# Kernel optimization log

Hardware: AMD Instinct MI355X
Metric: run time of the kernel (lower is better)

The kernel has to match this reference:

```python
import jax, jax.numpy as jnp
import numpy as np

NUM_HEADS = 16
HEAD_DIM = 64
WINDOW = 512
D_MODEL = NUM_HEADS * HEAD_DIM
BATCH = 2
SEQ = 2048


def setup_inputs() -> dict:
    key = jax.random.key(0)
    k1, k2, k3 = jax.random.split(key, 3)
    x = jax.random.normal(k1, (BATCH, SEQ, D_MODEL), dtype=jnp.float32)
    # Dense layer params (lecun_normal-like scale for stability)
    qkv_kernel = jax.random.normal(k2, (D_MODEL, 3 * NUM_HEADS * HEAD_DIM), dtype=jnp.float32) / np.sqrt(D_MODEL)
    qkv_bias = jnp.zeros((3 * NUM_HEADS * HEAD_DIM,), dtype=jnp.float32)
    out_kernel = jax.random.normal(k3, (NUM_HEADS * HEAD_DIM, D_MODEL), dtype=jnp.float32) / np.sqrt(D_MODEL)
    out_bias = jnp.zeros((D_MODEL,), dtype=jnp.float32)
    return {"x": x, "qkv_kernel": qkv_kernel, "qkv_bias": qkv_bias,
            "out_kernel": out_kernel, "out_bias": out_bias}


def reference(x, qkv_kernel, qkv_bias, out_kernel, out_bias):
    b, s, d = x.shape
    qkv = x @ qkv_kernel + qkv_bias                       # (b, s, 3*H*hd)
    qkv = qkv.reshape(b, s, 3, NUM_HEADS, HEAD_DIM)
    q = qkv[:, :, 0].transpose(0, 2, 1, 3)                # (b, H, s, hd)
    k = qkv[:, :, 1].transpose(0, 2, 1, 3)
    v = qkv[:, :, 2].transpose(0, 2, 1, 3)
    scale = 1.0 / jnp.sqrt(jnp.float32(HEAD_DIM)).astype(x.dtype)
    scores = jnp.einsum('bhqd,bhkd->bhqk', q, k) * scale  # (b, H, s, s)
    rows = jnp.arange(s)[:, None]
    cols = jnp.arange(s)[None, :]
    window_mask = (rows - cols >= 0) & (rows - cols < WINDOW)
    scores = jnp.where(window_mask[None, None], scores, jnp.asarray(-1e9, scores.dtype))
    attn = jax.nn.softmax(scores, axis=-1)
    out = jnp.einsum('bhqk,bhkd->bhqd', attn, v)          # (b, H, s, hd)
    out = out.transpose(0, 2, 1, 3).reshape(b, s, -1)
    return out @ out_kernel + out_bias
```

## Files before the change

kernel.cpp:

```cpp
#include <hip/hip_runtime.h>
#include <cstdint>
#include <cstddef>

#define NUM_HEADS 16
#define HEAD_DIM  64
#define WINDOW    512
#define D_MODEL   1024
#define BATCH     2
#define SEQ       2048
#define MTOT      (BATCH*SEQ)
#define NQKV      (3*D_MODEL)

typedef short bf16x8 __attribute__((ext_vector_type(8)));
typedef float f32x4  __attribute__((ext_vector_type(4)));

__device__ __forceinline__ f32x4 mfma16(bf16x8 a, bf16x8 b, f32x4 c) {
  return __builtin_amdgcn_mfma_f32_16x16x32_bf16(a, b, c, 0, 0, 0);
}

__device__ __forceinline__ unsigned short f2bf(float f) {
  unsigned int u = __float_as_uint(f);
  u += 0x7fffu + ((u >> 16) & 1u);
  return (unsigned short)(u >> 16);
}
__device__ __forceinline__ float bf2f(unsigned short b) {
  return __uint_as_float(((unsigned int)b) << 16);
}

__device__ __forceinline__ void gld16(const unsigned short* g, unsigned short* l) {
  __builtin_amdgcn_global_load_lds(
      (const __attribute__((address_space(1))) unsigned int*)g,
      (__attribute__((address_space(3))) unsigned int*)l, 16, 0, 0);
}

__global__ __launch_bounds__(256) void prep_kernel(const float* __restrict__ x,
                                                   const float* __restrict__ qkv_w,
                                                   const float* __restrict__ out_w,
                                                   unsigned short* __restrict__ Xb,
                                                   unsigned short* __restrict__ Wq,
                                                   unsigned short* __restrict__ Wo) {
  __shared__ float tile[32][33];
  const int bid = blockIdx.x, t = threadIdx.x;
  if (bid < 4096) {
    int i = (bid * 256 + t) * 4;
    float4 v = *(const float4*)(x + i);
    ushort4 o;
    o.x = f2bf(v.x); o.y = f2bf(v.y); o.z = f2bf(v.z); o.w = f2bf(v.w);
    *(ushort4*)(Xb + i) = o;
    return;
  }
  const float* in; unsigned short* out; int R, C, bx, by;
  if (bid < 7168) { int b2 = bid - 4096; in = qkv_w; out = Wq; R = D_MODEL; C = NQKV; bx = b2 % 96; by = b2 / 96; }
  else            { int b2 = bid - 7168; in = out_w; out = Wo; R = D_MODEL; C = D_MODEL; bx = b2 & 31; by = b2 >> 5; }
  int tx = t & 31, ty = t >> 5;
  int c0 = bx * 32, r0 = by * 32;
#pragma unroll
  for (int i = 0; i < 32; i += 8)
    tile[ty + i][tx] = in[(size_t)(r0 + ty + i) * C + c0 + tx];
  __syncthreads();
#pragma unroll
  for (int i = 0; i < 32; i += 8)
    out[(size_t)(c0 + ty + i) * R + r0 + tx] = f2bf(tile[tx][ty + i]);
}

template<bool SWAP, int K>
__device__ __forceinline__ void gemm_mainloop512(const unsigned short* __restrict__ A,
                                                 const unsigned short* __restrict__ Bt,
                                                 int m0, int n0,
                                                 unsigned short* sA, unsigned short* sB,
                                                 f32x4 (&acc)[2][4]) {
  const int t = threadIdx.x;
  const int lane = t & 63, wave = t >> 6;
  const int wr = wave >> 1, wc = wave & 1;
  const int lhi = lane >> 4, llo = lane & 15;
  f32x4 zero = {0.f, 0.f, 0.f, 0.f};
#pragma unroll
  for (int i = 0; i < 2; ++i)
#pragma unroll
    for (int j = 0; j < 4; ++j) acc[i][j] = zero;

  const int cswz = (((t & 3) ^ ((t >> 3) & 3)) << 3);
  const unsigned short* gA = A  + (size_t)(m0 + (t >> 2)) * K + cswz;
  const unsigned short* gB = Bt + (size_t)(n0 + (t >> 2)) * K + cswz;
  const int ldsT = t * 8;
  const int rsw  = (lhi ^ ((llo >> 1) & 3)) * 8;
  const int aoff = (wr * 32 + llo) * 32 + rsw;
  const int boff = (wc * 64 + llo) * 32 + rsw;
  constexpr int nIter = K / 32;

  auto stage = [&](int s) {
    unsigned short* dA = sA + (s % 3) * 4096;
    unsigned short* dB = sB + (s % 3) * 4096;
    gld16(gA + s * 32, dA + ldsT);
    gld16(gB + s * 32, dB + ldsT);
  };

  stage(0);
  stage(1);
#pragma unroll
  for (int it = 0; it < nIter; ++it) {
    if (it + 1 < nIter) asm volatile("s_waitcnt vmcnt(2)\n\ts_barrier" ::: "memory");
    else                asm volatile("s_waitcnt vmcnt(0)\n\ts_barrier" ::: "memory");
    if (it + 2 < nIter) stage(it + 2);
    const unsigned short* cA = sA + (it % 3) * 4096;
    const unsigned short* cB = sB + (it % 3) * 4096;
    bf16x8 af[2], bfr[4];
#pragma unroll
    for (int i = 0; i < 2; ++i) af[i]  = *(const bf16x8*)(cA + aoff + i * 512);
#pragma unroll
    for (int j = 0; j < 4; ++j)  bfr[j] = *(const bf16x8*)(cB + boff + j * 512);
#pragma unroll
    for (int i = 0; i < 2; ++i)
#pragma unroll
      for (int j = 0; j < 4; ++j)
        acc[i][j] = SWAP ? mfma16(bfr[j], af[i], acc[i][j])
                         : mfma16(af[i], bfr[j], acc[i][j]);
  }
}

__global__ __launch_bounds__(512, 6) void qkv_gemm_kernel(const unsigned short* __restrict__ Xb,
                                                          const unsigned short* __restrict__ Wt,
                                                          const float* __restrict__ bias,
                                                          unsigned short* __restrict__ Qw,
                                                          unsigned short* __restrict__ Kw,
                                                          unsigned short* __restrict__ Vtw) {
  __shared__ __align__(16) unsigned short sA[3][128 * 32];
  __shared__ __align__(16) unsigned short sB[3][128 * 32];
  f32x4 acc[2][4];
  const int m0 = blockIdx.y * 128, n0 = blockIdx.x * 128;
  const int t = threadIdx.x, lane = t & 63, wave = t >> 6;
  const int wr = wave >> 1, wc = wave & 1, lhi = lane >> 4, llo = lane & 15;

  if (n0 < 2048) {
    gemm_mainloop512<false, D_MODEL>(Xb, Wt, m0, n0, sA[0], sB[0], acc);
    const int c = n0 >> 10;
    unsigned short* __restrict__ Dst = (c == 0) ? Qw : Kw;
    const float qs = (c == 0) ? 0.125f : 1.0f;
#pragma unroll
    for (int ti = 0; ti < 2; ++ti) {
#pragma unroll
      for (int tj = 0; tj < 4; ++tj) {
        int n = n0 + wc * 64 + tj * 16 + llo;
        float bv = bias[n];
        int h = (n >> 6) & 15, d = n & 63;
#pragma unroll
        for (int r = 0; r < 4; ++r) {
          int m = m0 + wr * 32 + ti * 16 + lhi * 4 + r;
          int b = m >> 11, s = m & 2047;
          int bh = b * 16 + h;
          Dst[((size_t)(bh * 2048 + s)) * 64 + d] = f2bf((acc[ti][tj][r] + bv) * qs);
        }
      }
    }
  } else {
    gemm_mainloop512<true, D_MODEL>(Xb, Wt, m0, n0, sA[0], sB[0], acc);
#pragma unroll
    for (int ti = 0; ti < 2; ++ti) {
      int m = m0 + wr * 32 + ti * 16 + llo;
      int b = m >> 11, s = m & 2047;
#pragma unroll
      for (int tj = 0; tj < 4; ++tj) {
        int nb = n0 + wc * 64 + tj * 16 + lhi * 4;
        float4 bv = *(const float4*)(bias + nb);
        int h = (nb >> 6) & 15, dbase = nb & 63;
        int bh = b * 16 + h;
        float bvr[4] = {bv.x, bv.y, bv.z, bv.w};
#pragma unroll
        for (int r = 0; r < 4; ++r)
          Vtw[(size_t)(bh * 64 + dbase + r) * 2048 + s] = f2bf(acc[ti][tj][r] + bvr[r]);
      }
    }
  }
}

__global__ __launch_bounds__(512) void attn_kernel(const unsigned short* __restrict__ Qw,
                                                   const unsigned short* __restrict__ Kw,
                                                   const unsigned short* __restrict__ Vtw,
                                                   unsigned short* __restrict__ AO) {
  __shared__ __align__(16) unsigned short sK[3][64 * 64];
  __shared__ __align__(16) unsigned short sV[3][64 * 64];
  __shared__ __align__(16) unsigned short sP[8][16 * 72];
  const int t = threadIdx.x, lane = t & 63, wave = t >> 6;
  const int lhi = lane >> 4, llo = lane & 15;
  const int bh = blockIdx.x;
  const int q0 = (15 - blockIdx.y) << 7;
  const unsigned short* Qb = Qw  + (size_t)bh * 2048 * 64;
  const unsigned short* Kb = Kw  + (size_t)bh * 2048 * 64;
  const unsigned short* Vb = Vtw + (size_t)bh * 64 * 2048;

  const int qw = q0 + wave * 16;
  const int qrow = qw + llo;
  bf16x8 qf0 = *(const bf16x8*)(Qb + (size_t)qrow * 64 + lhi * 8);
  bf16x8 qf1 = *(const bf16x8*)(Qb + (size_t)qrow * 64 + 32 + lhi * 8);

  const int srow = t >> 3;
  const int scol = ((t & 7) ^ (srow & 7)) * 8;
  const int cpos  = (lhi ^ (llo & 7)) * 8;
  const int cposx = cpos ^ 32;

  float m_i = -1e30f, l_i = 0.f;
  f32x4 o[4];
  f32x4 zero = {0.f, 0.f, 0.f, 0.f};
#pragma unroll
  for (int td = 0; td < 4; ++td) o[td] = zero;

  const int kt_lo = (q0 > 511) ? ((q0 - 511) >> 6) : 0;
  const int kt_hi = (q0 + 127) >> 6;

  auto stageKV = [&](int j) {
    const int k0 = j << 6;
    unsigned short* dK = sK[j % 3];
    unsigned short* dV = sV[j % 3];
    gld16(Kb + (size_t)(k0 + srow) * 64 + scol, dK + t * 8);
    gld16(Vb + (size_t)srow * 2048 + k0 + scol, dV + t * 8);
  };

  stageKV(kt_lo);
  stageKV(kt_lo + 1);

  for (int kt = kt_lo; kt <= kt_hi; ++kt) {
    if (kt < kt_hi) asm volatile("s_waitcnt vmcnt(2)\n\ts_barrier" ::: "memory");
    else            asm volatile("s_waitcnt vmcnt(0)\n\ts_barrier" ::: "memory");
    if (kt + 2 <= kt_hi) stageKV(kt + 2);
    const int k0 = kt << 6;
    if (k0 > qw + 15 || k0 + 63 < qw - (WINDOW - 1)) continue;

    const unsigned short* bK = sK[kt % 3];
    const unsigned short* bV = sV[kt % 3];

    f32x4 st[4];
#pragma unroll
    for (int tk = 0; tk < 4; ++tk) {
      const unsigned short* kr = bK + (tk * 16 + llo) * 64;
      bf16x8 kf0 = *(const bf16x8*)(kr + cpos);
      bf16x8 kf1 = *(const bf16x8*)(kr + cposx);
      f32x4 z = zero;
      z = mfma16(kf0, qf0, z);
      z = mfma16(kf1, qf1, z);
      st[tk] = z;
    }

    const bool interior = (k0 >= qw - (WINDOW - 1 - 15)) && (k0 + 63 <= qw);
    const int kb = k0 + lhi * 4;
    float mx = -1e30f;
    if (interior) {
#pragma unroll
      for (int tk = 0; tk < 4; ++tk)
#pragma unroll
        for (int r = 0; r < 4; ++r) mx = fmaxf(mx, st[tk][r]);
    } else {
#pragma unroll
      for (int tk = 0; tk < 4; ++tk)
#pragma unroll
        for (int r = 0; r < 4; ++r) {
          int key = kb + tk * 16 + r;
          bool ok = (key <= qrow) && (qrow - key < WINDOW);
          float s = ok ? st[tk][r] : -1e30f;
          st[tk][r] = s;
          mx = fmaxf(mx, s);
        }
    }
    mx = fmaxf(mx, __shfl_xor(mx, 16));
    mx = fmaxf(mx, __shfl_xor(mx, 32));
    float mn = fmaxf(m_i, mx);
    float a  = __expf(m_i - mn);
    float rs = 0.f;
    unsigned short* pw = &sP[wave][llo * 72];
#pragma unroll
    for (int tk = 0; tk < 4; ++tk) {
      ushort4 pb;
      pb.x = f2bf(__expf(st[tk][0] - mn));
      pb.y = f2bf(__expf(st[tk][1] - mn));
      pb.z = f2bf(__expf(st[tk][2] - mn));
      pb.w = f2bf(__expf(st[tk][3] - mn));
      *(ushort4*)(pw + tk * 16 + lhi * 4) = pb;
      rs += bf2f(pb.x) + bf2f(pb.y) + bf2f(pb.z) + bf2f(pb.w);
    }
    rs += __shfl_xor(rs, 16);
    rs += __shfl_xor(rs, 32);
    l_i = l_i * a + rs;
    m_i = mn;

    float aR[4];
#pragma unroll
    for (int r = 0; r < 4; ++r) aR[r] = __shfl(a, lhi * 4 + r);
#pragma unroll
    for (int td = 0; td < 4; ++td)
#pragma unroll
      for (int r = 0; r < 4; ++r) o[td][r] *= aR[r];

    bf16x8 pf0 = *(const bf16x8*)(pw + lhi * 8);
    bf16x8 pf1 = *(const bf16x8*)(pw + 32 + lhi * 8);
#pragma unroll
    for (int td = 0; td < 4; ++td) {
      const unsigned short* vr = bV + (td * 16 + llo) * 64;
      bf16x8 vf0 = *(const bf16x8*)(vr + cpos);
      bf16x8 vf1 = *(const bf16x8*)(vr + cposx);
      o[td] = mfma16(pf0, vf0, o[td]);
      o[td] = mfma16(pf1, vf1, o[td]);
    }
  }

  float lR[4];
#pragma unroll
  for (int r = 0; r < 4; ++r) lR[r] = 1.f / __shfl(l_i, lhi * 4 + r);
  const int b = bh >> 4, h = bh & 15;
#pragma unroll
  for (int td = 0; td < 4; ++td)
#pragma unroll
    for (int r = 0; r < 4; ++r) {
      int qr = q0 + wave * 16 + lhi * 4 + r;
      AO[(size_t)(b * 2048 + qr) * 1024 + h * 64 + td * 16 + llo] = f2bf(o[td][r] * lR[r]);
    }
}

__global__ __launch_bounds__(512, 2) void out_gemm_kernel(const unsigned short* __restrict__ AO,
                                                          const unsigned short* __restrict__ Wt,
                                                          const float* __restrict__ bias,
                                                          float* __restrict__ out) {
  __shared__ __align__(16) unsigned short sA[3][128 * 32];
  __shared__ __align__(16) unsigned short sB[3][128 * 32];
  f32x4 acc[2][4];
  const int m0 = blockIdx.y * 128, n0 = blockIdx.x * 128;
  gemm_mainloop512<false, D_MODEL>(AO, Wt, m0, n0, sA[0], sB[0], acc);

  const int t = threadIdx.x, lane = t & 63, wave = t >> 6;
  const int wr = wave >> 1, wc = wave & 1, lhi = lane >> 4, llo = lane & 15;
#pragma unroll
  for (int ti = 0; ti < 2; ++ti)
#pragma unroll
    for (int tj = 0; tj < 4; ++tj) {
      int n = n0 + wc * 64 + tj * 16 + llo;
      float bv = bias[n];
#pragma unroll
      for (int r = 0; r < 4; ++r) {
        int m = m0 + wr * 32 + ti * 16 + lhi * 4 + r;
        out[(size_t)m * D_MODEL + n] = acc[ti][tj][r] + bv;
      }
    }
}

extern "C" void kernel_launch(void* const* d_in, const int* in_sizes, int n_in,
                              void* d_out, int out_size, void* d_ws, size_t ws_size,
                              hipStream_t stream) {
  const float* x      = (const float*)d_in[0];
  const float* qkv_w  = (const float*)d_in[1];
  const float* qkv_b  = (const float*)d_in[2];
  const float* out_w  = (const float*)d_in[3];
  const float* out_b  = (const float*)d_in[4];
  float* out = (float*)d_out;
  char* ws = (char*)d_ws;

  unsigned short* Xb  = (unsigned short*)(ws);
  unsigned short* Wq  = (unsigned short*)(ws + ((size_t)8  << 20));
  unsigned short* Wo  = (unsigned short*)(ws + ((size_t)14 << 20));
  unsigned short* Qw  = (unsigned short*)(ws + ((size_t)16 << 20));
  unsigned short* Kw  = (unsigned short*)(ws + ((size_t)24 << 20));
  unsigned short* Vtw = (unsigned short*)(ws + ((size_t)32 << 20));
  unsigned short* AO  = (unsigned short*)(ws + ((size_t)40 << 20));

  prep_kernel<<<8192, 256, 0, stream>>>(x, qkv_w, out_w, Xb, Wq, Wo);
  qkv_gemm_kernel<<<dim3(NQKV / 128, MTOT / 128), 512, 0, stream>>>(Xb, Wq, qkv_b, Qw, Kw, Vtw);
  attn_kernel<<<dim3(BATCH * NUM_HEADS, SEQ / 128), 512, 0, stream>>>(Qw, Kw, Vtw, AO);
  out_gemm_kernel<<<dim3(D_MODEL / 128, MTOT / 128), 512, 0, stream>>>(AO, Wo, out_b, out);
}
```

Baseline: 163.8 us.

## Shrink attention and output-GEMM tiles to raise block count and occupancy

The attention kernel now uses 64-query blocks of 4 waves instead of 128-query blocks of 8 waves. That doubles the grid and removes the extra key tiles each block had to cover for its taller query range. K/V staging moves from a triple buffer to a double buffer with two loads per thread, plus a trailing barrier before the next tile is staged. The output projection gets its own mainloop with 128x64 tiles, more blocks, and a higher occupancy target. The smaller tiles reuse less data per block and the extra barrier adds synchronization.

```diff
diff --git a/kernel.cpp b/kernel.cpp
--- a/kernel.cpp
+++ b/kernel.cpp
@@ -173,17 +173,17 @@
   }
 }
 
-__global__ __launch_bounds__(512) void attn_kernel(const unsigned short* __restrict__ Qw,
+__global__ __launch_bounds__(256) void attn_kernel(const unsigned short* __restrict__ Qw,
                                                    const unsigned short* __restrict__ Kw,
                                                    const unsigned short* __restrict__ Vtw,
                                                    unsigned short* __restrict__ AO) {
-  __shared__ __align__(16) unsigned short sK[3][64 * 64];
-  __shared__ __align__(16) unsigned short sV[3][64 * 64];
-  __shared__ __align__(16) unsigned short sP[8][16 * 72];
+  __shared__ __align__(16) unsigned short sK[2][64 * 64];
+  __shared__ __align__(16) unsigned short sV[2][64 * 64];
+  __shared__ __align__(16) unsigned short sP[4][16 * 72];
   const int t = threadIdx.x, lane = t & 63, wave = t >> 6;
   const int lhi = lane >> 4, llo = lane & 15;
   const int bh = blockIdx.x;
-  const int q0 = (15 - blockIdx.y) << 7;
+  const int q0 = (31 - blockIdx.y) << 6;
   const unsigned short* Qb = Qw  + (size_t)bh * 2048 * 64;
   const unsigned short* Kb = Kw  + (size_t)bh * 2048 * 64;
   const unsigned short* Vb = Vtw + (size_t)bh * 64 * 2048;
@@ -195,6 +195,7 @@
 
   const int srow = t >> 3;
   const int scol = ((t & 7) ^ (srow & 7)) * 8;
+  const int scol2 = ((t & 7) ^ ((srow + 32) & 7)) * 8;
   const int cpos  = (lhi ^ (llo & 7)) * 8;
   const int cposx = cpos ^ 32;
 
@@ -205,100 +206,105 @@
   for (int td = 0; td < 4; ++td) o[td] = zero;
 
   const int kt_lo = (q0 > 511) ? ((q0 - 511) >> 6) : 0;
-  const int kt_hi = (q0 + 127) >> 6;
+  const int kt_hi = q0 >> 6;
 
   auto stageKV = [&](int j) {
     const int k0 = j << 6;
-    unsigned short* dK = sK[j % 3];
-    unsigned short* dV = sV[j % 3];
-    gld16(Kb + (size_t)(k0 + srow) * 64 + scol, dK + t * 8);
-    gld16(Vb + (size_t)srow * 2048 + k0 + scol, dV + t * 8);
+    unsigned short* dK = sK[j & 1];
+    unsigned short* dV = sV[j & 1];
+    gld16(Kb + (size_t)(k0 + srow) * 64 + scol,       dK + t * 8);
+    gld16(Kb + (size_t)(k0 + srow + 32) * 64 + scol2, dK + 2048 + t * 8);
+    gld16(Vb + (size_t)srow * 2048 + k0 + scol,         dV + t * 8);
+    gld16(Vb + (size_t)(srow + 32) * 2048 + k0 + scol2, dV + 2048 + t * 8);
   };
 
   stageKV(kt_lo);
   stageKV(kt_lo + 1);
 
   for (int kt = kt_lo; kt <= kt_hi; ++kt) {
-    if (kt < kt_hi) asm volatile("s_waitcnt vmcnt(2)\n\ts_barrier" ::: "memory");
+    if (kt < kt_hi) asm volatile("s_waitcnt vmcnt(4)\n\ts_barrier" ::: "memory");
     else            asm volatile("s_waitcnt vmcnt(0)\n\ts_barrier" ::: "memory");
+    const int k0 = kt << 6;
+
+    if (!(k0 > qw + 15 || k0 + 63 < qw - (WINDOW - 1))) {
+      const unsigned short* bK = sK[kt & 1];
+      const unsigned short* bV = sV[kt & 1];
+
+      f32x4 st[4];
+#pragma unroll
+      for (int tk = 0; tk < 4; ++tk) {
+        const unsigned short* kr = bK + (tk * 16 + llo) * 64;
+        bf16x8 kf0 = *(const bf16x8*)(kr + cpos);
+        bf16x8 kf1 = *(const bf16x8*)(kr + cposx);
+        f32x4 z = zero;
+        z = mfma16(kf0, qf0, z);
+        z = mfma16(kf1, qf1, z);
+        st[tk] = z;
+      }
+
+      const bool interior = (k0 >= qw - (WINDOW - 16)) && (k0 + 63 <= qw);
+      const int kb = k0 + lhi * 4;
+      float mx = -1e30f;
+      if (interior) {
+#pragma unroll
+        for (int tk = 0; tk < 4; ++tk)
+#pragma unroll
+          for (int r = 0; r < 4; ++r) mx = fmaxf(mx, st[tk][r]);
+      } else {
+#pragma unroll
+        for (int tk = 0; tk < 4; ++tk)
+#pragma unroll
+          for (int r = 0; r < 4; ++r) {
+            int key = kb + tk * 16 + r;
+            bool ok = (key <= qrow) && (qrow - key < WINDOW);
+            float s = ok ? st[tk][r] : -1e30f;
+            st[tk][r] = s;
+            mx = fmaxf(mx, s);
+          }
+      }
+      mx = fmaxf(mx, __shfl_xor(mx, 16));
+      mx = fmaxf(mx, __shfl_xor(mx, 32));
+      float mn = fmaxf(m_i, mx);
+      float a  = __expf(m_i - mn);
+      float rs = 0.f;
+      unsigned short* pw = &sP[wave][llo * 72];
+#pragma unroll
+      for (int tk = 0; tk < 4; ++tk) {
+        ushort4 pb;
+        pb.x = f2bf(__expf(st[tk][0] - mn));
+        pb.y = f2bf(__expf(st[tk][1] - mn));
+        pb.z = f2bf(__expf(st[tk][2] - mn));
+        pb.w = f2bf(__expf(st[tk][3] - mn));
+        *(ushort4*)(pw + tk * 16 + lhi * 4) = pb;
+        rs += bf2f(pb.x) + bf2f(pb.y) + bf2f(pb.z) + bf2f(pb.w);
+      }
+      rs += __shfl_xor(rs, 16);
+      rs += __shfl_xor(rs, 32);
+      l_i = l_i * a + rs;
+      m_i = mn;
+
+      float aR[4];
+#pragma unroll
+      for (int r = 0; r < 4; ++r) aR[r] = __shfl(a, lhi * 4 + r);
+#pragma unroll
+      for (int td = 0; td < 4; ++td)
+#pragma unroll
+        for (int r = 0; r < 4; ++r) o[td][r] *= aR[r];
+
+      bf16x8 pf0 = *(const bf16x8*)(pw + lhi * 8);
+      bf16x8 pf1 = *(const bf16x8*)(pw + 32 + lhi * 8);
+#pragma unroll
+      for (int td = 0; td < 4; ++td) {
+        const unsigned short* vr = bV + (td * 16 + llo) * 64;
+        bf16x8 vf0 = *(const bf16x8*)(vr + cpos);
+        bf16x8 vf1 = *(const bf16x8*)(vr + cposx);
+        o[td] = mfma16(pf0, vf0, o[td]);
+        o[td] = mfma16(pf1, vf1, o[td]);
+      }
+    }
+
+    asm volatile("s_barrier" ::: "memory");
     if (kt + 2 <= kt_hi) stageKV(kt + 2);
-    const int k0 = kt << 6;
-    if (k0 > qw + 15 || k0 + 63 < qw - (WINDOW - 1)) continue;
-
-    const unsigned short* bK = sK[kt % 3];
-    const unsigned short* bV = sV[kt % 3];
-
-    f32x4 st[4];
-#pragma unroll
-    for (int tk = 0; tk < 4; ++tk) {
-      const unsigned short* kr = bK + (tk * 16 + llo) * 64;
-      bf16x8 kf0 = *(const bf16x8*)(kr + cpos);
-      bf16x8 kf1 = *(const bf16x8*)(kr + cposx);
-      f32x4 z = zero;
-      z = mfma16(kf0, qf0, z);
-      z = mfma16(kf1, qf1, z);
-      st[tk] = z;
-    }
-
-    const bool interior = (k0 >= qw - (WINDOW - 1 - 15)) && (k0 + 63 <= qw);
-    const int kb = k0 + lhi * 4;
-    float mx = -1e30f;
-    if (interior) {
-#pragma unroll
-      for (int tk = 0; tk < 4; ++tk)
-#pragma unroll
-        for (int r = 0; r < 4; ++r) mx = fmaxf(mx, st[tk][r]);
-    } else {
-#pragma unroll
-      for (int tk = 0; tk < 4; ++tk)
-#pragma unroll
-        for (int r = 0; r < 4; ++r) {
-          int key = kb + tk * 16 + r;
-          bool ok = (key <= qrow) && (qrow - key < WINDOW);
-          float s = ok ? st[tk][r] : -1e30f;
-          st[tk][r] = s;
-          mx = fmaxf(mx, s);
-        }
-    }
-    mx = fmaxf(mx, __shfl_xor(mx, 16));
-    mx = fmaxf(mx, __shfl_xor(mx, 32));
-    float mn = fmaxf(m_i, mx);
-    float a  = __expf(m_i - mn);
-    float rs = 0.f;
-    unsigned short* pw = &sP[wave][llo * 72];
-#pragma unroll
-    for (int tk = 0; tk < 4; ++tk) {
-      ushort4 pb;
-      pb.x = f2bf(__expf(st[tk][0] - mn));
-      pb.y = f2bf(__expf(st[tk][1] - mn));
-      pb.z = f2bf(__expf(st[tk][2] - mn));
-      pb.w = f2bf(__expf(st[tk][3] - mn));
-      *(ushort4*)(pw + tk * 16 + lhi * 4) = pb;
-      rs += bf2f(pb.x) + bf2f(pb.y) + bf2f(pb.z) + bf2f(pb.w);
-    }
-    rs += __shfl_xor(rs, 16);
-    rs += __shfl_xor(rs, 32);
-    l_i = l_i * a + rs;
-    m_i = mn;
-
-    float aR[4];
-#pragma unroll
-    for (int r = 0; r < 4; ++r) aR[r] = __shfl(a, lhi * 4 + r);
-#pragma unroll
-    for (int td = 0; td < 4; ++td)
-#pragma unroll
-      for (int r = 0; r < 4; ++r) o[td][r] *= aR[r];
-
-    bf16x8 pf0 = *(const bf16x8*)(pw + lhi * 8);
-    bf16x8 pf1 = *(const bf16x8*)(pw + 32 + lhi * 8);
-#pragma unroll
-    for (int td = 0; td < 4; ++td) {
-      const unsigned short* vr = bV + (td * 16 + llo) * 64;
-      bf16x8 vf0 = *(const bf16x8*)(vr + cpos);
-      bf16x8 vf1 = *(const bf16x8*)(vr + cposx);
-      o[td] = mfma16(pf0, vf0, o[td]);
-      o[td] = mfma16(pf1, vf1, o[td]);
-    }
   }
 
   float lR[4];
@@ -314,23 +320,66 @@
     }
 }
 
-__global__ __launch_bounds__(512, 2) void out_gemm_kernel(const unsigned short* __restrict__ AO,
+__global__ __launch_bounds__(512, 6) void out_gemm_kernel(const unsigned short* __restrict__ AO,
                                                           const unsigned short* __restrict__ Wt,
                                                           const float* __restrict__ bias,
                                                           float* __restrict__ out) {
   __shared__ __align__(16) unsigned short sA[3][128 * 32];
-  __shared__ __align__(16) unsigned short sB[3][128 * 32];
-  f32x4 acc[2][4];
-  const int m0 = blockIdx.y * 128, n0 = blockIdx.x * 128;
-  gemm_mainloop512<false, D_MODEL>(AO, Wt, m0, n0, sA[0], sB[0], acc);
-
+  __shared__ __align__(16) unsigned short sB[3][64 * 32];
+  f32x4 acc[2][2];
+  const int m0 = blockIdx.y * 128, n0 = blockIdx.x * 64;
   const int t = threadIdx.x, lane = t & 63, wave = t >> 6;
   const int wr = wave >> 1, wc = wave & 1, lhi = lane >> 4, llo = lane & 15;
+  f32x4 zero = {0.f, 0.f, 0.f, 0.f};
+#pragma unroll
+  for (int i = 0; i < 2; ++i)
+#pragma unroll
+    for (int j = 0; j < 2; ++j) acc[i][j] = zero;
+
+  const int cswz = (((t & 3) ^ ((t >> 3) & 3)) << 3);
+  const unsigned short* gA = AO + (size_t)(m0 + (t >> 2)) * D_MODEL + cswz;
+  const unsigned short* gB = Wt + (size_t)(n0 + (t >> 2)) * D_MODEL + cswz;
+  const int ldsT = t * 8;
+  const int rsw  = (lhi ^ ((llo >> 1) & 3)) * 8;
+  const int aoff = (wr * 32 + llo) * 32 + rsw;
+  const int boff = (wc * 32 + llo) * 32 + rsw;
+  constexpr int nIter = D_MODEL / 32;
+
+  auto stage = [&](int s) {
+    gld16(gA + s * 32, sA[s % 3] + ldsT);
+    if (t < 256) gld16(gB + s * 32, sB[s % 3] + ldsT);
+  };
+
+  stage(0);
+  stage(1);
+#pragma unroll
+  for (int it = 0; it < nIter; ++it) {
+    if (it + 1 < nIter) {
+      if (wave < 4) asm volatile("s_waitcnt vmcnt(2)\n\ts_barrier" ::: "memory");
+      else          asm volatile("s_waitcnt vmcnt(1)\n\ts_barrier" ::: "memory");
+    } else {
+      asm volatile("s_waitcnt vmcnt(0)\n\ts_barrier" ::: "memory");
+    }
+    if (it + 2 < nIter) stage(it + 2);
+    const unsigned short* cA = sA[it % 3];
+    const unsigned short* cB = sB[it % 3];
+    bf16x8 af[2], bfr[2];
+#pragma unroll
+    for (int i = 0; i < 2; ++i) af[i]  = *(const bf16x8*)(cA + aoff + i * 512);
+#pragma unroll
+    for (int j = 0; j < 2; ++j) bfr[j] = *(const bf16x8*)(cB + boff + j * 512);
+#pragma unroll
+    for (int i = 0; i < 2; ++i)
+#pragma unroll
+      for (int j = 0; j < 2; ++j)
+        acc[i][j] = mfma16(af[i], bfr[j], acc[i][j]);
+  }
+
 #pragma unroll
   for (int ti = 0; ti < 2; ++ti)
 #pragma unroll
-    for (int tj = 0; tj < 4; ++tj) {
-      int n = n0 + wc * 64 + tj * 16 + llo;
+    for (int tj = 0; tj < 2; ++tj) {
+      int n = n0 + wc * 32 + tj * 16 + llo;
       float bv = bias[n];
 #pragma unroll
       for (int r = 0; r < 4; ++r) {
@@ -361,6 +410,6 @@
 
   prep_kernel<<<8192, 256, 0, stream>>>(x, qkv_w, out_w, Xb, Wq, Wo);
   qkv_gemm_kernel<<<dim3(NQKV / 128, MTOT / 128), 512, 0, stream>>>(Xb, Wq, qkv_b, Qw, Kw, Vtw);
-  attn_kernel<<<dim3(BATCH * NUM_HEADS, SEQ / 128), 512, 0, stream>>>(Qw, Kw, Vtw, AO);
-  out_gemm_kernel<<<dim3(D_MODEL / 128, MTOT / 128), 512, 0, stream>>>(AO, Wo, out_b, out);
-}
+  attn_kernel<<<dim3(BATCH * NUM_HEADS, SEQ / 64), 256, 0, stream>>>(Qw, Kw, Vtw, AO);
+  out_gemm_kernel<<<dim3(D_MODEL / 64, MTOT / 128), 512, 0, stream>>>(AO, Wo, out_b, out);
+}
```

Result: slower. 170.4 us (+4.0%).
